# Kernel optimization log

Measured on AMD Instinct MI355X. Metric: run time of the kernel, lower is better.

Reference implementation:

```python
import jax, jax.numpy as jnp
import numpy as np

N_NODES = 1048576
N_EDGES = 4 * N_NODES

def _mlp(h, w1, b1, w2, b2):
    return jax.nn.relu(h @ w1 + b1) @ w2 + b2

def setup_inputs() -> dict:
    key = jax.random.key(0)
    ks = jax.random.split(key, 12)
    def glorot(k, shape):
        fan_in, fan_out = shape
        lim = np.sqrt(6.0 / (fan_in + fan_out)).astype(np.float32)
        return jax.random.uniform(k, shape, jnp.float32, -lim, lim)
    x = jax.random.normal(ks[0], (N_NODES, 3), jnp.float32)
    edge_index = jax.random.randint(ks[1], (2, N_EDGES), 0, N_NODES, jnp.int64 if jax.config.jax_enable_x64 else jnp.int32)
    edge_attr = jax.random.normal(ks[2], (N_EDGES, 1), jnp.float32)
    u = jax.random.normal(ks[3], (1, 3), jnp.float32)
    batch = jnp.zeros((N_NODES,), jnp.int32)
    return {
        'x': x, 'edge_index': edge_index, 'edge_attr': edge_attr, 'u': u, 'batch': batch,
        'w1a': glorot(ks[4], (4, 20)), 'b1a': jnp.zeros((20,), jnp.float32),
        'w1b': glorot(ks[5], (20, 3)), 'b1b': jnp.zeros((3,), jnp.float32),
        'w2a': glorot(ks[6], (6, 20)), 'b2a': jnp.zeros((20,), jnp.float32),
        'w2b': glorot(ks[7], (20, 3)), 'b2b': jnp.zeros((3,), jnp.float32),
    }

def reference(x, edge_index, edge_attr, u, batch, w1a, b1a, w1b, b1b, w2a, b2a, w2b, b2b):
    row, col = edge_index[0], edge_index[1]
    n = x.shape[0]
    # gather source node feats, concat edge attr -> [E,4]
    h = jnp.concatenate([x[row], edge_attr], axis=1)
    h = _mlp(h, w1a, b1a, w1b, b1b)                    # [E,3]
    # scatter-mean over destination nodes
    s = jax.ops.segment_sum(h, col, num_segments=n)    # [N,3]
    cnt = jax.ops.segment_sum(jnp.ones((h.shape[0],), h.dtype), col, num_segments=n)
    agg = s / jnp.maximum(cnt, 1.0)[:, None]
    out = _mlp(jnp.concatenate([x, agg], axis=1), w2a, b2a, w2b, b2b)  # [N,3]
    fac = jnp.sqrt(jnp.sum(out ** 2, axis=1, keepdims=True))
    return out / fac
```

## Files before the change

kernel.cpp:

```cpp
#include <hip/hip_runtime.h>


#define SEG  4096
#define P1BT 256
#define P1BI (SEG / P1BT)
#define BKSH 12
#define BKN  4096
#define NBK  256
#define PFXW 257
#define P2T  1024

typedef unsigned long long u64x2 __attribute__((ext_vector_type(2)));

union HCvt { _Float16 h; unsigned short u; };

__device__ __forceinline__ float h2f(unsigned short u) {
    HCvt c; c.u = u; return (float)c.h;
}

__device__ __forceinline__ void mlp1_eval(
    float in0, float in1, float in2, float in3,
    const float* sw1a, const float* sb1a, const float* sw1b, const float* sb1b,
    float& o0, float& o1, float& o2)
{
    float h1[20];
#pragma unroll
    for (int j = 0; j < 20; ++j) {
        float v = sb1a[j];
        v = fmaf(in0, sw1a[0 * 20 + j], v);
        v = fmaf(in1, sw1a[1 * 20 + j], v);
        v = fmaf(in2, sw1a[2 * 20 + j], v);
        v = fmaf(in3, sw1a[3 * 20 + j], v);
        h1[j] = v > 0.f ? v : 0.f;
    }
    o0 = sb1b[0]; o1 = sb1b[1]; o2 = sb1b[2];
#pragma unroll
    for (int j = 0; j < 20; ++j) {
        o0 = fmaf(h1[j], sw1b[j * 3 + 0], o0);
        o1 = fmaf(h1[j], sw1b[j * 3 + 1], o1);
        o2 = fmaf(h1[j], sw1b[j * 3 + 2], o2);
    }
    o0 = fminf(fmaxf(o0, -8.0f), 8.0f - 2.0f / 2048.0f);
    o1 = fminf(fmaxf(o1, -8.0f), 8.0f - 2.0f / 2048.0f);
    o2 = fminf(fmaxf(o2, -8.0f), 8.0f - 2.0f / 1024.0f);
}

__device__ __forceinline__ unsigned long long payload_pack(float o0, float o1, float o2)
{
    const unsigned long long q0 = (unsigned int)__float2int_rn((o0 + 8.0f) * 2048.0f);
    const unsigned long long q1 = (unsigned int)__float2int_rn((o1 + 8.0f) * 2048.0f);
    const unsigned long long q2 = (unsigned int)__float2int_rn((o2 + 8.0f) * 1024.0f);
    return (q0 << 12) | (q1 << 27) | (q2 << 42);
}

__device__ __forceinline__ unsigned long long acc_pack(float o0, float o1, float o2)
{
    const unsigned long long q0 = (unsigned int)__float2int_rn((o0 + 8.0f) * 2048.0f);
    const unsigned long long q1 = (unsigned int)__float2int_rn((o1 + 8.0f) * 2048.0f);
    const unsigned long long q2 = (unsigned int)__float2int_rn((o2 + 8.0f) * 1024.0f);
    return 1ULL | (q0 << 5) | (q1 << 25) | (q2 << 45);
}

__device__ __forceinline__ void mlp2_store(
    unsigned long long q, const float* __restrict__ x, float* __restrict__ out,
    int n, const float* sw2a, const float* sb2a, const float* sw2b, const float* sb2b)
{
    const float cnt = (float)(unsigned int)(q & 31ULL);
    const float f0 = (float)(unsigned int)((q >> 5)  & 0xFFFFFULL);
    const float f1 = (float)(unsigned int)((q >> 25) & 0xFFFFFULL);
    const float f2 = (float)(unsigned int)(q >> 45);
    const float s0 = f0 * (1.0f / 2048.0f) - 8.0f * cnt;
    const float s1 = f1 * (1.0f / 2048.0f) - 8.0f * cnt;
    const float s2 = f2 * (1.0f / 1024.0f) - 8.0f * cnt;
    const float invc = 1.0f / fmaxf(cnt, 1.0f);

    const float in0 = x[n * 3 + 0];
    const float in1 = x[n * 3 + 1];
    const float in2 = x[n * 3 + 2];
    const float in3 = s0 * invc;
    const float in4 = s1 * invc;
    const float in5 = s2 * invc;

    float h1[20];
#pragma unroll
    for (int j = 0; j < 20; ++j) {
        float v = sb2a[j];
        v = fmaf(in0, sw2a[0 * 20 + j], v);
        v = fmaf(in1, sw2a[1 * 20 + j], v);
        v = fmaf(in2, sw2a[2 * 20 + j], v);
        v = fmaf(in3, sw2a[3 * 20 + j], v);
        v = fmaf(in4, sw2a[4 * 20 + j], v);
        v = fmaf(in5, sw2a[5 * 20 + j], v);
        h1[j] = v > 0.f ? v : 0.f;
    }
    float o0 = sb2b[0], o1 = sb2b[1], o2 = sb2b[2];
#pragma unroll
    for (int j = 0; j < 20; ++j) {
        o0 = fmaf(h1[j], sw2b[j * 3 + 0], o0);
        o1 = fmaf(h1[j], sw2b[j * 3 + 1], o1);
        o2 = fmaf(h1[j], sw2b[j * 3 + 2], o2);
    }
    const float inv = 1.0f / sqrtf(o0 * o0 + o1 * o1 + o2 * o2);
    out[n * 3 + 0] = o0 * inv;
    out[n * 3 + 1] = o1 * inv;
    out[n * 3 + 2] = o2 * inv;
}

__global__ __launch_bounds__(256) void pack_x_kernel(
    const float* __restrict__ x, ushort4* __restrict__ xp, int N)
{
    const int n = blockIdx.x * 256 + threadIdx.x;
    if (n >= N) return;
    HCvt c0, c1, c2;
    c0.h = (_Float16)x[n * 3 + 0];
    c1.h = (_Float16)x[n * 3 + 1];
    c2.h = (_Float16)x[n * 3 + 2];
    ushort4 r; r.x = c0.u; r.y = c1.u; r.z = c2.u; r.w = 0;
    xp[n] = r;
}

__global__ __launch_bounds__(256) void p1a_kernel(
    const unsigned long long* __restrict__ xp,
    const int*   __restrict__ edge_index,
    const float* __restrict__ edge_attr,
    const float* __restrict__ w1a, const float* __restrict__ b1a,
    const float* __restrict__ w1b, const float* __restrict__ b1b,
    unsigned long long* __restrict__ recs,
    int e_base, int e_end, int E)
{
    __shared__ float sw1a[80], sb1a[20], sw1b[60], sb1b[3];
    const int t = threadIdx.x;
    if (t < 80) sw1a[t] = w1a[t];
    if (t < 20) sb1a[t] = b1a[t];
    if (t < 60) sw1b[t] = w1b[t];
    if (t < 3)  sb1b[t] = b1b[t];
    __syncthreads();

    const int e = e_base + blockIdx.x * 256 + t;
    if (e >= e_end) return;

    const int row = __builtin_nontemporal_load(edge_index + e);
    const float attr = __builtin_nontemporal_load(edge_attr + e);
    const unsigned long long px = xp[row];
    float o0, o1, o2;
    mlp1_eval(h2f((unsigned short)px), h2f((unsigned short)(px >> 16)),
              h2f((unsigned short)(px >> 32)), attr,
              sw1a, sb1a, sw1b, sb1b, o0, o1, o2);
    __builtin_nontemporal_store(payload_pack(o0, o1, o2), recs + e);
}

__global__ __launch_bounds__(P1BT) void p1b_kernel(
    const int* __restrict__ edge_index,
    unsigned long long* __restrict__ recs,
    unsigned short* __restrict__ pfx_tr,
    int E, int nsegs)
{
    __shared__ unsigned int hist[NBK];
    __shared__ unsigned int sc[NBK];
    __shared__ unsigned int pfx[PFXW];
    __shared__ __align__(16) unsigned long long svals[SEG];
    const int t = threadIdx.x;
    hist[t] = 0;
    __syncthreads();

    const int s = blockIdx.x;
    const int base = s * SEG;

    unsigned int col8[P1BI];
#pragma unroll
    for (int i = 0; i < P1BI; ++i) {
        const int e = base + i * P1BT + t;
        if (e < E) {
            const unsigned int c = (unsigned int)edge_index[E + e];
            col8[i] = c;
            atomicAdd(&hist[c >> BKSH], 1u);
        } else {
            col8[i] = 0xFFFFFFFFu;
        }
    }
    __syncthreads();

    sc[t] = hist[t];
    __syncthreads();
#pragma unroll
    for (int off = 1; off < NBK; off <<= 1) {
        const unsigned int u = (t >= off) ? sc[t - off] : 0u;
        __syncthreads();
        sc[t] += u;
        __syncthreads();
    }
    pfx[t + 1] = sc[t];
    if (t == 0) pfx[0] = 0;
    hist[t] = 0;
    __syncthreads();

    pfx_tr[(size_t)t * nsegs + s] = (unsigned short)pfx[t];
    if (t == 0) pfx_tr[(size_t)NBK * nsegs + s] = (unsigned short)pfx[NBK];

#pragma unroll
    for (int i = 0; i < P1BI; ++i) {
        const unsigned int c = col8[i];
        if (c == 0xFFFFFFFFu) continue;
        const int e = base + i * P1BT + t;
        const unsigned long long rec =
            recs[e] | (unsigned long long)(c & (BKN - 1));
        const unsigned int bkt = c >> BKSH;
        const unsigned int r = atomicAdd(&hist[bkt], 1u);
        svals[pfx[bkt] + r] = rec;
    }
    __syncthreads();

    unsigned long long* gv = recs + (size_t)base;
#pragma unroll
    for (int k = t; k < SEG; k += P1BT) gv[k] = svals[k];
}

__global__ __launch_bounds__(P2T) void p2_kernel(
    const float* __restrict__ x,
    const unsigned short* __restrict__ pfx_tr,
    const unsigned long long* __restrict__ vals,
    const float* __restrict__ w2a, const float* __restrict__ b2a,
    const float* __restrict__ w2b, const float* __restrict__ b2b,
    float* __restrict__ out,
    int N, int nsegs)
{
    __shared__ float sw2a[120], sb2a[20], sw2b[60], sb2b[3];
    __shared__ unsigned long long acc[BKN];
    const int t = threadIdx.x;
    if (t < 120) sw2a[t] = w2a[t];
    if (t < 20)  sb2a[t] = b2a[t];
    if (t < 60)  sw2b[t] = w2b[t];
    if (t < 3)   sb2b[t] = b2b[t];
#pragma unroll
    for (int k = 0; k < BKN / P2T; ++k) acc[k * P2T + t] = 0ULL;
    __syncthreads();

    const int b = blockIdx.x;
    const int wave = t >> 6;
    const int lane = t & 63;
    const int sub  = lane >> 4;
    const int sl   = lane & 15;
    const unsigned short* rowa = pfx_tr + (size_t)b * nsegs;
    const unsigned short* rowb = pfx_tr + (size_t)(b + 1) * nsegs;

    for (int sg = wave * 4; sg < nsegs; sg += (P2T / 64) * 4) {
        const int s = sg + sub;
        if (s < nsegs) {
            const unsigned int pa = rowa[s];
            const unsigned int pb = rowb[s];
            const size_t base = (size_t)s * SEG;
            for (unsigned int i = pa + sl; i < pb; i += 16) {
                const unsigned long long rec = vals[base + i];
                const unsigned int c = (unsigned int)(rec & 0xFFFULL);
                const unsigned long long q0 = (rec >> 12) & 0x7FFFULL;
                const unsigned long long q1 = (rec >> 27) & 0x7FFFULL;
                const unsigned long long q2 = (rec >> 42) & 0x3FFFULL;
                const unsigned long long add =
                    1ULL | (q0 << 5) | (q1 << 25) | (q2 << 45);
                atomicAdd(&acc[c], add);
            }
        }
    }
    __syncthreads();

    const int node0 = b * BKN;
#pragma unroll
    for (int k = 0; k < BKN / P2T; ++k) {
        const int n = node0 + k * P2T + t;
        if (n >= N) continue;
        mlp2_store(acc[k * P2T + t], x, out, n, sw2a, sb2a, sw2b, sb2b);
    }
}

__global__ __launch_bounds__(256) void edge_kernel_fb(
    const float* __restrict__ x, const int* __restrict__ edge_index,
    const float* __restrict__ edge_attr,
    const float* __restrict__ w1a, const float* __restrict__ b1a,
    const float* __restrict__ w1b, const float* __restrict__ b1b,
    unsigned long long* __restrict__ acc, int E)
{
    __shared__ float sw1a[80], sb1a[20], sw1b[60], sb1b[3];
    const int t = threadIdx.x;
    if (t < 80) sw1a[t] = w1a[t];
    if (t < 20) sb1a[t] = b1a[t];
    if (t < 60) sw1b[t] = w1b[t];
    if (t < 3)  sb1b[t] = b1b[t];
    __syncthreads();
    const int e = blockIdx.x * 256 + t;
    if (e >= E) return;
    const int row = edge_index[e];
    const int col = edge_index[E + e];
    float o0, o1, o2;
    mlp1_eval(x[row * 3 + 0], x[row * 3 + 1], x[row * 3 + 2], edge_attr[e],
              sw1a, sb1a, sw1b, sb1b, o0, o1, o2);
    atomicAdd(acc + col, acc_pack(o0, o1, o2));
}

__global__ __launch_bounds__(256) void node_kernel_fb(
    const float* __restrict__ x, const unsigned long long* __restrict__ acc,
    const float* __restrict__ w2a, const float* __restrict__ b2a,
    const float* __restrict__ w2b, const float* __restrict__ b2b,
    float* __restrict__ out, int N)
{
    __shared__ float sw2a[120], sb2a[20], sw2b[60], sb2b[3];
    const int t = threadIdx.x;
    if (t < 120) sw2a[t] = w2a[t];
    if (t < 20)  sb2a[t] = b2a[t];
    if (t < 60)  sw2b[t] = w2b[t];
    if (t < 3)   sb2b[t] = b2b[t];
    __syncthreads();
    const int n = blockIdx.x * 256 + threadIdx.x;
    if (n >= N) return;
    mlp2_store(acc[n], x, out, n, sw2a, sb2a, sw2b, sb2b);
}

extern "C" void kernel_launch(void* const* d_in, const int* in_sizes, int n_in,
                              void* d_out, int out_size, void* d_ws, size_t ws_size,
                              hipStream_t stream) {
    const float* x          = (const float*)d_in[0];
    const int*   edge_index = (const int*)  d_in[1];
    const float* edge_attr  = (const float*)d_in[2];
    const float* w1a = (const float*)d_in[5];
    const float* b1a = (const float*)d_in[6];
    const float* w1b = (const float*)d_in[7];
    const float* b1b = (const float*)d_in[8];
    const float* w2a = (const float*)d_in[9];
    const float* b2a = (const float*)d_in[10];
    const float* w2b = (const float*)d_in[11];
    const float* b2b = (const float*)d_in[12];

    const int N = in_sizes[0] / 3;
    const int E = in_sizes[2];

    const int nbuckets = (N + BKN - 1) / BKN;
    const int nsegs = (E + SEG - 1) / SEG;

    const size_t xp_bytes   = (size_t)N * sizeof(unsigned long long);
    const size_t recs_off   = (xp_bytes + 255) & ~(size_t)255;
    const size_t recs_bytes = (size_t)nsegs * SEG * sizeof(unsigned long long);
    const size_t pfx_off    = (recs_off + recs_bytes + 255) & ~(size_t)255;
    const size_t need       = pfx_off + (size_t)PFXW * nsegs * sizeof(unsigned short);

    const bool fast = (nbuckets <= NBK) && (ws_size >= need);

    if (fast) {
        unsigned long long* xp = (unsigned long long*)d_ws;
        unsigned long long* recs = (unsigned long long*)((char*)d_ws + recs_off);
        unsigned short* pfx_tr = (unsigned short*)((char*)d_ws + pfx_off);

        pack_x_kernel<<<(N + 255) / 256, 256, 0, stream>>>(
            x, (ushort4*)xp, N);

        const int Eh = ((E / 2) + 255) & ~255;
        p1a_kernel<<<(Eh + 255) / 256, 256, 0, stream>>>(
            xp, edge_index, edge_attr, w1a, b1a, w1b, b1b, recs, 0, Eh, E);
        p1a_kernel<<<((E - Eh) + 255) / 256, 256, 0, stream>>>(
            xp, edge_index, edge_attr, w1a, b1a, w1b, b1b, recs, Eh, E, E);

        p1b_kernel<<<nsegs, P1BT, 0, stream>>>(
            edge_index, recs, pfx_tr, E, nsegs);

        p2_kernel<<<nbuckets, P2T, 0, stream>>>(
            x, pfx_tr, recs, w2a, b2a, w2b, b2b, (float*)d_out, N, nsegs);
    } else {
        unsigned long long* acc = (unsigned long long*)d_ws;
        hipMemsetAsync(acc, 0, (size_t)N * sizeof(unsigned long long), stream);
        edge_kernel_fb<<<(E + 255) / 256, 256, 0, stream>>>(
            x, edge_index, edge_attr, w1a, b1a, w1b, b1b, acc, E);
        node_kernel_fb<<<(N + 255) / 256, 256, 0, stream>>>(
            x, acc, w2a, b2a, w2b, b2b, (float*)d_out, N);
    }
}
```

Measured before the change: 230.3 us.

## Fuse all phases into one cooperative persistent kernel with grid syncs

Replaces the four-kernel sequence (pack, edge MLP, per-segment bucket sort, per-bucket aggregation plus node MLP) with a single cooperative kernel. It uses 1024-thread blocks sized to occupancy and separates the phases with grid.sync(). The goal is to remove launch gaps and tail idle time between phases, at the cost of grid-wide barrier overhead. Occupancy also drops because the 1024-thread blocks carry the large shared arrays, and grid-stride loops replace one-block-per-item mapping. The fallback path also merges the two half-range p1a launches into one.

```diff
diff --git a/kernel.cpp b/kernel.cpp
--- a/kernel.cpp
+++ b/kernel.cpp
@@ -1,16 +1,17 @@
 #include <hip/hip_runtime.h>
+#include <hip/hip_cooperative_groups.h>
+
+namespace cg = cooperative_groups;
 
 
 #define SEG  4096
 #define P1BT 256
-#define P1BI (SEG / P1BT)
 #define BKSH 12
 #define BKN  4096
 #define NBK  256
 #define PFXW 257
 #define P2T  1024
-
-typedef unsigned long long u64x2 __attribute__((ext_vector_type(2)));
+#define FT   1024
 
 union HCvt { _Float16 h; unsigned short u; };
 
@@ -106,6 +107,165 @@
     out[n * 3 + 2] = o2 * inv;
 }
 
+__global__ __launch_bounds__(FT) void fused_kernel(
+    const float* __restrict__ x,
+    const int* __restrict__ edge_index,
+    const float* __restrict__ edge_attr,
+    const float* __restrict__ w1a, const float* __restrict__ b1a,
+    const float* __restrict__ w1b, const float* __restrict__ b1b,
+    const float* __restrict__ w2a, const float* __restrict__ b2a,
+    const float* __restrict__ w2b, const float* __restrict__ b2b,
+    unsigned long long* __restrict__ xp,
+    unsigned long long* __restrict__ recs,
+    unsigned short* __restrict__ pfx_tr,
+    float* __restrict__ out,
+    int N, int E, int nsegs, int nbuckets)
+{
+    cg::grid_group grid = cg::this_grid();
+    const int t = threadIdx.x;
+    const int nthreads = (int)(gridDim.x * FT);
+    const int gtid = (int)(blockIdx.x * FT) + t;
+
+    __shared__ float sw1a[80], sb1a[20], sw1b[60], sb1b[3];
+    __shared__ float sw2a[120], sb2a[20], sw2b[60], sb2b[3];
+    __shared__ unsigned int hist[NBK];
+    __shared__ unsigned int sc[NBK];
+    __shared__ unsigned int pfx[PFXW];
+    __shared__ __align__(16) unsigned long long svals[SEG];
+
+    if (t < 80)  sw1a[t] = w1a[t];
+    if (t < 20)  sb1a[t] = b1a[t];
+    if (t < 60)  sw1b[t] = w1b[t];
+    if (t < 3)   sb1b[t] = b1b[t];
+    if (t < 120) sw2a[t] = w2a[t];
+    if (t >= 128 && t < 148) sb2a[t - 128] = b2a[t - 128];
+    if (t >= 192 && t < 252) sw2b[t - 192] = w2b[t - 192];
+    if (t >= 252 && t < 255) sb2b[t - 252] = b2b[t - 252];
+    __syncthreads();
+
+    for (int n = gtid; n < N; n += nthreads) {
+        HCvt c0, c1, c2;
+        c0.h = (_Float16)x[n * 3 + 0];
+        c1.h = (_Float16)x[n * 3 + 1];
+        c2.h = (_Float16)x[n * 3 + 2];
+        xp[n] = (unsigned long long)c0.u |
+                ((unsigned long long)c1.u << 16) |
+                ((unsigned long long)c2.u << 32);
+    }
+    grid.sync();
+
+    for (int e = gtid; e < E; e += nthreads) {
+        const int row = edge_index[e];
+        const float attr = __builtin_nontemporal_load(edge_attr + e);
+        const unsigned long long px = xp[row];
+        float o0, o1, o2;
+        mlp1_eval(h2f((unsigned short)px), h2f((unsigned short)(px >> 16)),
+                  h2f((unsigned short)(px >> 32)), attr,
+                  sw1a, sb1a, sw1b, sb1b, o0, o1, o2);
+        recs[e] = payload_pack(o0, o1, o2);
+    }
+    grid.sync();
+
+    for (int s = blockIdx.x; s < nsegs; s += (int)gridDim.x) {
+        const int base = s * SEG;
+        if (t < NBK) hist[t] = 0;
+        __syncthreads();
+
+        unsigned int col4[SEG / FT];
+#pragma unroll
+        for (int i = 0; i < SEG / FT; ++i) {
+            const int e = base + i * FT + t;
+            if (e < E) {
+                const unsigned int c = (unsigned int)edge_index[E + e];
+                col4[i] = c;
+                atomicAdd(&hist[c >> BKSH], 1u);
+            } else {
+                col4[i] = 0xFFFFFFFFu;
+            }
+        }
+        __syncthreads();
+
+        if (t < NBK) sc[t] = hist[t];
+        __syncthreads();
+#pragma unroll
+        for (int off = 1; off < NBK; off <<= 1) {
+            unsigned int u = 0;
+            if (t < NBK && t >= off) u = sc[t - off];
+            __syncthreads();
+            if (t < NBK) sc[t] += u;
+            __syncthreads();
+        }
+        if (t < NBK) { pfx[t + 1] = sc[t]; hist[t] = 0; }
+        if (t == 0) pfx[0] = 0;
+        __syncthreads();
+
+        if (t < NBK) pfx_tr[(size_t)t * nsegs + s] = (unsigned short)pfx[t];
+        if (t == 0)  pfx_tr[(size_t)NBK * nsegs + s] = (unsigned short)pfx[NBK];
+
+#pragma unroll
+        for (int i = 0; i < SEG / FT; ++i) {
+            const unsigned int c = col4[i];
+            if (c == 0xFFFFFFFFu) continue;
+            const int e = base + i * FT + t;
+            const unsigned long long rec =
+                recs[e] | (unsigned long long)(c & (BKN - 1));
+            const unsigned int bkt = c >> BKSH;
+            const unsigned int r = atomicAdd(&hist[bkt], 1u);
+            svals[pfx[bkt] + r] = rec;
+        }
+        __syncthreads();
+
+        unsigned long long* gv = recs + (size_t)base;
+        for (int k = t; k < SEG; k += FT) gv[k] = svals[k];
+        __syncthreads();
+    }
+    grid.sync();
+
+    unsigned long long* acc = svals;
+    for (int b = blockIdx.x; b < nbuckets; b += (int)gridDim.x) {
+#pragma unroll
+        for (int k = 0; k < BKN / FT; ++k) acc[k * FT + t] = 0ULL;
+        __syncthreads();
+
+        const int wave = t >> 6;
+        const int lane = t & 63;
+        const int sub  = lane >> 4;
+        const int sl   = lane & 15;
+        const unsigned short* rowa = pfx_tr + (size_t)b * nsegs;
+        const unsigned short* rowb = pfx_tr + (size_t)(b + 1) * nsegs;
+
+        for (int sg = wave * 4; sg < nsegs; sg += (FT / 64) * 4) {
+            const int s = sg + sub;
+            if (s < nsegs) {
+                const unsigned int pa = rowa[s];
+                const unsigned int pb = rowb[s];
+                const size_t sbase = (size_t)s * SEG;
+                for (unsigned int i = pa + sl; i < pb; i += 16) {
+                    const unsigned long long rec = recs[sbase + i];
+                    const unsigned int c = (unsigned int)(rec & 0xFFFULL);
+                    const unsigned long long q0 = (rec >> 12) & 0x7FFFULL;
+                    const unsigned long long q1 = (rec >> 27) & 0x7FFFULL;
+                    const unsigned long long q2 = (rec >> 42) & 0x3FFFULL;
+                    const unsigned long long add =
+                        1ULL | (q0 << 5) | (q1 << 25) | (q2 << 45);
+                    atomicAdd(&acc[c], add);
+                }
+            }
+        }
+        __syncthreads();
+
+        const int node0 = b * BKN;
+#pragma unroll
+        for (int k = 0; k < BKN / FT; ++k) {
+            const int n = node0 + k * FT + t;
+            if (n < N) mlp2_store(acc[k * FT + t], x, out, n,
+                                  sw2a, sb2a, sw2b, sb2b);
+        }
+        __syncthreads();
+    }
+}
+
+
 __global__ __launch_bounds__(256) void pack_x_kernel(
     const float* __restrict__ x, ushort4* __restrict__ xp, int N)
 {
@@ -126,7 +286,7 @@
     const float* __restrict__ w1a, const float* __restrict__ b1a,
     const float* __restrict__ w1b, const float* __restrict__ b1b,
     unsigned long long* __restrict__ recs,
-    int e_base, int e_end, int E)
+    int E)
 {
     __shared__ float sw1a[80], sb1a[20], sw1b[60], sb1b[3];
     const int t = threadIdx.x;
@@ -136,8 +296,8 @@
     if (t < 3)  sb1b[t] = b1b[t];
     __syncthreads();
 
-    const int e = e_base + blockIdx.x * 256 + t;
-    if (e >= e_end) return;
+    const int e = blockIdx.x * 256 + t;
+    if (e >= E) return;
 
     const int row = __builtin_nontemporal_load(edge_index + e);
     const float attr = __builtin_nontemporal_load(edge_attr + e);
@@ -166,9 +326,9 @@
     const int s = blockIdx.x;
     const int base = s * SEG;
 
-    unsigned int col8[P1BI];
-#pragma unroll
-    for (int i = 0; i < P1BI; ++i) {
+    unsigned int col8[SEG / P1BT];
+#pragma unroll
+    for (int i = 0; i < SEG / P1BT; ++i) {
         const int e = base + i * P1BT + t;
         if (e < E) {
             const unsigned int c = (unsigned int)edge_index[E + e];
@@ -198,7 +358,7 @@
     if (t == 0) pfx_tr[(size_t)NBK * nsegs + s] = (unsigned short)pfx[NBK];
 
 #pragma unroll
-    for (int i = 0; i < P1BI; ++i) {
+    for (int i = 0; i < SEG / P1BT; ++i) {
         const unsigned int c = col8[i];
         if (c == 0xFFFFFFFFu) continue;
         const int e = base + i * P1BT + t;
@@ -348,20 +508,54 @@
         unsigned long long* recs = (unsigned long long*)((char*)d_ws + recs_off);
         unsigned short* pfx_tr = (unsigned short*)((char*)d_ws + pfx_off);
 
-        pack_x_kernel<<<(N + 255) / 256, 256, 0, stream>>>(
-            x, (ushort4*)xp, N);
-
-        const int Eh = ((E / 2) + 255) & ~255;
-        p1a_kernel<<<(Eh + 255) / 256, 256, 0, stream>>>(
-            xp, edge_index, edge_attr, w1a, b1a, w1b, b1b, recs, 0, Eh, E);
-        p1a_kernel<<<((E - Eh) + 255) / 256, 256, 0, stream>>>(
-            xp, edge_index, edge_attr, w1a, b1a, w1b, b1b, recs, Eh, E, E);
-
-        p1b_kernel<<<nsegs, P1BT, 0, stream>>>(
-            edge_index, recs, pfx_tr, E, nsegs);
-
-        p2_kernel<<<nbuckets, P2T, 0, stream>>>(
-            x, pfx_tr, recs, w2a, b2a, w2b, b2b, (float*)d_out, N, nsegs);
+        static int coop_grid = -2;
+        if (coop_grid == -2) {
+            coop_grid = 0;
+            hipDeviceProp_t prop;
+            if (hipGetDeviceProperties(&prop, 0) == hipSuccess &&
+                prop.cooperativeLaunch) {
+                int nb = 0;
+                if (hipOccupancyMaxActiveBlocksPerMultiprocessor(
+                        &nb, (const void*)fused_kernel, FT, 0) == hipSuccess &&
+                    nb > 0) {
+                    coop_grid = nb * prop.multiProcessorCount;
+                }
+            }
+        }
+
+        bool launched = false;
+        if (coop_grid > 0) {
+            void* fx   = (void*)x;        void* fei  = (void*)edge_index;
+            void* fea  = (void*)edge_attr;
+            void* fw1a = (void*)w1a; void* fb1a = (void*)b1a;
+            void* fw1b = (void*)w1b; void* fb1b = (void*)b1b;
+            void* fw2a = (void*)w2a; void* fb2a = (void*)b2a;
+            void* fw2b = (void*)w2b; void* fb2b = (void*)b2b;
+            void* fxp  = (void*)xp;  void* frec = (void*)recs;
+            void* fpfx = (void*)pfx_tr; void* fout = d_out;
+            int   fN = N, fE = E, fns = nsegs, fnb = nbuckets;
+            void* args[] = { &fx, &fei, &fea,
+                             &fw1a, &fb1a, &fw1b, &fb1b,
+                             &fw2a, &fb2a, &fw2b, &fb2b,
+                             &fxp, &frec, &fpfx, &fout,
+                             &fN, &fE, &fns, &fnb };
+            const hipError_t err = hipLaunchCooperativeKernel(
+                (const void*)fused_kernel, dim3(coop_grid), dim3(FT),
+                args, 0, stream);
+            launched = (err == hipSuccess);
+            if (!launched) coop_grid = 0;
+        }
+
+        if (!launched) {
+            pack_x_kernel<<<(N + 255) / 256, 256, 0, stream>>>(
+                x, (ushort4*)xp, N);
+            p1a_kernel<<<(E + 255) / 256, 256, 0, stream>>>(
+                xp, edge_index, edge_attr, w1a, b1a, w1b, b1b, recs, E);
+            p1b_kernel<<<nsegs, P1BT, 0, stream>>>(
+                edge_index, recs, pfx_tr, E, nsegs);
+            p2_kernel<<<nbuckets, P2T, 0, stream>>>(
+                x, pfx_tr, recs, w2a, b2a, w2b, b2b, (float*)d_out, N, nsegs);
+        }
     } else {
         unsigned long long* acc = (unsigned long long*)d_ws;
         hipMemsetAsync(acc, 0, (size_t)N * sizeof(unsigned long long), stream);
```

After: 226.2 us. Within noise of the previous version (-1.8%).
